# Kernel optimization log

Hardware: AMD Instinct MI355X
Metric: run time of the kernel (lower is better)

## Reference

```python
import jax, jax.numpy as jnp
import numpy as np

B, L, F = 512, 128, 300          # batch, cycles per sample, curve length
D_MODEL = 512
D_LLM = 4096
E = 8                            # num_experts
G = 2                            # num_general_experts
TOP_K = 2
P = TOP_K / E                    # top-p threshold = topK / num_experts
EPS = 1e-9


def setup_inputs() -> dict:
    key = jax.random.key(0)
    ks = jax.random.split(key, 8)
    s_in = 1.0 / np.sqrt(3 * F).astype(np.float32)   # torch Linear init bound
    s_g = 1.0 / np.sqrt(D_LLM).astype(np.float32)
    return {
        "cycle_curve_data": jax.random.normal(ks[0], (B, L, 3, F), jnp.float32),
        "DKP_embeddings": jax.random.normal(ks[1], (B, D_LLM), jnp.float32),
        "W_exp": jax.random.uniform(ks[2], (E, 3 * F, D_MODEL), jnp.float32, -s_in, s_in),
        "b_exp": jax.random.uniform(ks[3], (E, D_MODEL), jnp.float32, -s_in, s_in),
        "W_gen": jax.random.uniform(ks[4], (G, 3 * F, D_MODEL), jnp.float32, -s_in, s_in),
        "b_gen": jax.random.uniform(ks[5], (G, D_MODEL), jnp.float32, -s_in, s_in),
        "W_gate": jax.random.uniform(ks[6], (D_LLM, E), jnp.float32, -s_g, s_g),
        "b_gate": jax.random.uniform(ks[7], (E,), jnp.float32, -s_g, s_g),
    }


def top_p_mask(logits, p):
    # softmax -> sort desc -> cumsum < p (first always kept) -> scatter back
    probs = jax.nn.softmax(logits, axis=-1)
    order = jnp.argsort(-probs, axis=-1)
    cum = jnp.cumsum(jnp.take_along_axis(probs, order, axis=-1), axis=-1)
    m = (cum < p).at[:, 0].set(True)
    rows = jnp.arange(logits.shape[0])[:, None]
    return jnp.zeros(logits.shape, bool).at[rows, order].set(m)


def reference(cycle_curve_data, DKP_embeddings, W_exp, b_exp, W_gen, b_gen, W_gate, b_gate):
    Bsz, Ls = cycle_curve_data.shape[:2]
    x = cycle_curve_data.reshape(Bsz, Ls, -1)            # [B, L, 3F]  (Flatten(start_dim=2))

    # gate (eval path: no noisy gating)
    logits = DKP_embeddings @ W_gate + b_gate            # [B, E]
    mask = top_p_mask(logits, P)
    w = jax.nn.softmax(logits, axis=1) * mask            # masked gate probs
    w = w / (jnp.sum(w, axis=1, keepdims=True) + EPS)    # renormalize (zeros stay zero)

    # dense equivalent of per-expert gather -> Linear -> weighted scatter-combine:
    # tokens with w[b,e]==0 contribute nothing, matching the sparse dispatcher.
    expert_outs = jnp.einsum('blf,efd->ebld', x, W_exp) + b_exp[:, None, None, :]  # [E,B,L,D]
    combined = jnp.einsum('be,ebld->bld', w, expert_outs).astype(jnp.bfloat16)     # [B,L,D] bf16

    # general experts run over the full batch and accumulate (bf16 + f32 -> f32)
    gen = jnp.einsum('blf,gfd->bld', x, W_gen) + jnp.sum(b_gen, axis=0)            # [B,L,D]
    return combined + gen
```

## Files before the change

kernel.cpp:

```cpp
#include <hip/hip_runtime.h>
#include <stdint.h>

#define NB   512
#define NL   128
#define NK   900
#define NKP  928
#define NKT  29
#define ND   512
#define NDLLM 4096
#define NE   8

typedef __bf16 bf16x8 __attribute__((ext_vector_type(8)));
typedef float  f32x4  __attribute__((ext_vector_type(4)));

__device__ __forceinline__ unsigned short f2bf(float f) {
  union { float f; uint32_t u; } v; v.f = f;
  uint32_t u = v.u;
  return (unsigned short)((u + 0x7fffu + ((u >> 16) & 1u)) >> 16);
}

__global__ __launch_bounds__(256) void gate_kernel(
    const float* __restrict__ dkp,
    const float* __restrict__ Wg,
    const float* __restrict__ bg,
    int* __restrict__ eidx)
{
  const int b = blockIdx.x;
  const int t = threadIdx.x;
  float acc[8];
#pragma unroll
  for (int e = 0; e < 8; ++e) acc[e] = 0.f;
  const float* drow = dkp + (size_t)b * NDLLM;
  for (int k = t; k < NDLLM; k += 256) {
    float d = drow[k];
    const float4* w4 = (const float4*)(Wg + (size_t)k * 8);
    float4 w0 = w4[0], w1 = w4[1];
    acc[0] += d * w0.x; acc[1] += d * w0.y; acc[2] += d * w0.z; acc[3] += d * w0.w;
    acc[4] += d * w1.x; acc[5] += d * w1.y; acc[6] += d * w1.z; acc[7] += d * w1.w;
  }
#pragma unroll
  for (int e = 0; e < 8; ++e)
    for (int off = 32; off >= 1; off >>= 1)
      acc[e] += __shfl_down(acc[e], off, 64);

  __shared__ float red[4][8];
  const int wave = t >> 6, lane = t & 63;
  if (lane == 0) {
#pragma unroll
    for (int e = 0; e < 8; ++e) red[wave][e] = acc[e];
  }
  __syncthreads();
  if (t == 0) {
    float best = -1e30f; int bi = 0;
#pragma unroll
    for (int e = 0; e < 8; ++e) {
      float v = red[0][e] + red[1][e] + red[2][e] + red[3][e] + bg[e];
      if (v > best) { best = v; bi = e; }
    }
    eidx[b] = bi;
  }
}

__global__ __launch_bounds__(256) void pack_kernel(
    const float* __restrict__ Wexp,
    const float* __restrict__ Wgen,
    unsigned short* __restrict__ Wt)
{
  const int nt = blockIdx.x;
  const int kt = blockIdx.y;
  const int e  = blockIdx.z;
  const int k0 = kt * 32, n0 = nt * 64;
  __shared__ float tile[32][65];
  const int t = threadIdx.x;
#pragma unroll
  for (int i = 0; i < 8; ++i) {
    int idx = t + i * 256;
    int k = idx >> 6, n = idx & 63;
    int kg = k0 + k;
    float v = 0.f;
    if (kg < NK) {
      size_t off = (size_t)kg * ND + n0 + n;
      v = Wexp[(size_t)e * NK * ND + off] + Wgen[off] + Wgen[(size_t)NK * ND + off];
    }
    tile[k][n] = v;
  }
  __syncthreads();
#pragma unroll
  for (int i = 0; i < 8; ++i) {
    int idx = t + i * 256;
    int n = idx >> 5, k = idx & 31;
    Wt[((size_t)e * ND + n0 + n) * NKP + k0 + k] = f2bf(tile[k][n]);
  }
}

__global__ __launch_bounds__(256) void bias_kernel(
    const float* __restrict__ bexp, const float* __restrict__ bgen,
    float* __restrict__ btot)
{
  int i = blockIdx.x * 256 + threadIdx.x;
  int d = i & (ND - 1);
  btot[i] = bexp[i] + bgen[d] + bgen[ND + d];
}

__global__ __launch_bounds__(256) void gemm_kernel(
    const float* __restrict__ x,
    const unsigned short* __restrict__ Wt,
    const float* __restrict__ btot,
    const int* __restrict__ eidx,
    float* __restrict__ out)
{
  __shared__ unsigned short As[NL * 32];
  __shared__ unsigned short Bs[128 * 32];

  const int b  = blockIdx.y;
  const int nt = blockIdx.x;
  const int t  = threadIdx.x;
  const int lane = t & 63;
  const int w  = t >> 6;
  const int wm = (w >> 1) * 64;
  const int wn = (w & 1) * 64;
  const int ln = lane & 15;
  const int kq = lane >> 4;

  const int e = eidx[b];
  const float* xb = x + (size_t)b * NL * NK;
  const unsigned short* wtb = Wt + ((size_t)e * ND + (size_t)nt * 128) * NKP;

  f32x4 acc[4][4];
  const f32x4 zero = {0.f, 0.f, 0.f, 0.f};
#pragma unroll
  for (int i = 0; i < 4; ++i)
#pragma unroll
    for (int j = 0; j < 4; ++j) acc[i][j] = zero;

  const int al  = t >> 3;
  const int akc = t & 7;

  for (int kt = 0; kt < NKT; ++kt) {
    const int k0 = kt * 32;
    __syncthreads();

#pragma unroll
    for (int p = 0; p < 2; ++p) {
      int c = t + p * 256;
      int n = c >> 2, kc8 = c & 3;
      const unsigned short* src = wtb + (size_t)n * NKP + k0 + kc8 * 8;
      unsigned short* dst = &Bs[c * 8];
      __builtin_amdgcn_global_load_lds(
          (__attribute__((address_space(1))) void*)(void*)src,
          (__attribute__((address_space(3))) void*)dst, 16, 0, 0);
    }

#pragma unroll
    for (int p = 0; p < 4; ++p) {
      int l  = al + p * 32;
      int kg = k0 + akc * 4;
      ushort4 h;
      if (kg < NK) {
        const float4 v = *(const float4*)(xb + (size_t)l * NK + kg);
        h.x = f2bf(v.x); h.y = f2bf(v.y); h.z = f2bf(v.z); h.w = f2bf(v.w);
      } else {
        h.x = 0; h.y = 0; h.z = 0; h.w = 0;
      }
      *(ushort4*)&As[l * 32 + akc * 4] = h;
    }
    __syncthreads();

    bf16x8 af[4], bv[4];
#pragma unroll
    for (int mi = 0; mi < 4; ++mi)
      af[mi] = *(bf16x8*)&As[(wm + mi * 16 + ln) * 32 + kq * 8];
#pragma unroll
    for (int ni = 0; ni < 4; ++ni)
      bv[ni] = *(bf16x8*)&Bs[(wn + ni * 16 + ln) * 32 + kq * 8];
#pragma unroll
    for (int mi = 0; mi < 4; ++mi)
#pragma unroll
      for (int ni = 0; ni < 4; ++ni)
        acc[mi][ni] = __builtin_amdgcn_mfma_f32_16x16x32_bf16(
            af[mi], bv[ni], acc[mi][ni], 0, 0, 0);
  }

  const float* bt = btot + (size_t)e * ND;
  const int nb = nt * 128;
#pragma unroll
  for (int ni = 0; ni < 4; ++ni) {
    int ncol = nb + wn + ni * 16 + ln;
    float bias = bt[ncol];
#pragma unroll
    for (int mi = 0; mi < 4; ++mi) {
      int l0 = wm + mi * 16 + kq * 4;
      float* op = out + ((size_t)b * NL + l0) * ND + ncol;
#pragma unroll
      for (int r = 0; r < 4; ++r)
        op[(size_t)r * ND] = acc[mi][ni][r] + bias;
    }
  }
}

extern "C" void kernel_launch(void* const* d_in, const int* in_sizes, int n_in,
                              void* d_out, int out_size, void* d_ws, size_t ws_size,
                              hipStream_t stream) {
  const float* x     = (const float*)d_in[0];
  const float* dkp   = (const float*)d_in[1];
  const float* Wexp  = (const float*)d_in[2];
  const float* bexp  = (const float*)d_in[3];
  const float* Wgen  = (const float*)d_in[4];
  const float* bgen  = (const float*)d_in[5];
  const float* Wgate = (const float*)d_in[6];
  const float* bgate = (const float*)d_in[7];
  float* out = (float*)d_out;

  int*   eidx = (int*)d_ws;
  float* btot = (float*)((char*)d_ws + 2048);
  unsigned short* Wt = (unsigned short*)((char*)d_ws + 18432);

  gate_kernel<<<NB, 256, 0, stream>>>(dkp, Wgate, bgate, eidx);
  pack_kernel<<<dim3(8, NKT, NE), 256, 0, stream>>>(Wexp, Wgen, Wt);
  bias_kernel<<<16, 256, 0, stream>>>(bexp, bgen, btot);
  gemm_kernel<<<dim3(4, NB), 256, 0, stream>>>(x, Wt, btot, eidx, out);
}
```

Before: 592.2 us.

## Compute full D row per block with double-buffered register-staged LDS pipeline

The GEMM now assigns one block of 512 threads per batch sample, covering all 512 output columns, so each x tile is read and converted to bf16 once instead of four times. Global loads for the next K-step are issued into registers before the MFMA compute on the current LDS buffer, giving software pipelining with two LDS buffers. LDS rows are padded to a stride of 40 to reduce bank conflicts, and outputs use nontemporal stores. The costs are more accumulator registers per thread (128 floats), more LDS per block, a 2-blocks-per-CU launch bound, and a grid of only 512 blocks, which lowers occupancy and parallelism.

```diff
diff --git a/kernel.cpp b/kernel.cpp
--- a/kernel.cpp
+++ b/kernel.cpp
@@ -9,6 +9,7 @@
 #define ND   512
 #define NDLLM 4096
 #define NE   8
+#define ASTR 40
 
 typedef __bf16 bf16x8 __attribute__((ext_vector_type(8)));
 typedef float  f32x4  __attribute__((ext_vector_type(4)));
@@ -102,100 +103,122 @@
   btot[i] = bexp[i] + bgen[d] + bgen[ND + d];
 }
 
-__global__ __launch_bounds__(256) void gemm_kernel(
+__global__ __launch_bounds__(512, 2) void gemm_kernel(
     const float* __restrict__ x,
     const unsigned short* __restrict__ Wt,
     const float* __restrict__ btot,
     const int* __restrict__ eidx,
     float* __restrict__ out)
 {
-  __shared__ unsigned short As[NL * 32];
-  __shared__ unsigned short Bs[128 * 32];
-
-  const int b  = blockIdx.y;
-  const int nt = blockIdx.x;
-  const int t  = threadIdx.x;
+  __shared__ unsigned short As[2][NL * ASTR];
+  __shared__ unsigned short Bs[2][ND * ASTR];
+
+  const int b    = blockIdx.x;
+  const int t    = threadIdx.x;
   const int lane = t & 63;
-  const int w  = t >> 6;
-  const int wm = (w >> 1) * 64;
-  const int wn = (w & 1) * 64;
-  const int ln = lane & 15;
-  const int kq = lane >> 4;
+  const int w    = t >> 6;
+  const int wm   = (w >> 2) * 64;
+  const int wn   = (w & 3) * 128;
+  const int ln   = lane & 15;
+  const int kq   = lane >> 4;
 
   const int e = eidx[b];
   const float* xb = x + (size_t)b * NL * NK;
-  const unsigned short* wtb = Wt + ((size_t)e * ND + (size_t)nt * 128) * NKP;
-
-  f32x4 acc[4][4];
+  const unsigned short* wtb = Wt + (size_t)e * ND * NKP;
+
+  const int arow  = t >> 3;
+  const int acol  = t & 7;
+  const int brow  = t >> 2;
+  const int bslot = t & 3;
+
+  f32x4 acc[4][8];
   const f32x4 zero = {0.f, 0.f, 0.f, 0.f};
 #pragma unroll
-  for (int i = 0; i < 4; ++i)
-#pragma unroll
-    for (int j = 0; j < 4; ++j) acc[i][j] = zero;
-
-  const int al  = t >> 3;
-  const int akc = t & 7;
-
-  for (int kt = 0; kt < NKT; ++kt) {
-    const int k0 = kt * 32;
+  for (int mi = 0; mi < 4; ++mi)
+#pragma unroll
+    for (int ni = 0; ni < 8; ++ni) acc[mi][ni] = zero;
+
+  f32x4 aIn[2];
+  uint4 bIn[4];
+
+#define ISSUE_LOADS(K0)                                                       \
+  {                                                                           \
+    const int kg_ = (K0) + acol * 4;                                          \
+    if (kg_ < NK) {                                                           \
+      aIn[0] = *(const f32x4*)(xb + (size_t)arow * NK + kg_);                 \
+      aIn[1] = *(const f32x4*)(xb + (size_t)(arow + 64) * NK + kg_);          \
+    } else {                                                                  \
+      aIn[0] = zero; aIn[1] = zero;                                           \
+    }                                                                         \
+    const unsigned short* bsrc_ = wtb + (K0) + bslot * 8;                     \
+    _Pragma("unroll")                                                         \
+    for (int p = 0; p < 4; ++p)                                               \
+      bIn[p] = *(const uint4*)(bsrc_ + (size_t)(brow + p * 128) * NKP);       \
+  }
+
+#define WRITE_STAGE(BUF)                                                      \
+  {                                                                           \
+    _Pragma("unroll")                                                         \
+    for (int p = 0; p < 2; ++p) {                                             \
+      ushort4 h_;                                                             \
+      h_.x = f2bf(aIn[p][0]); h_.y = f2bf(aIn[p][1]);                         \
+      h_.z = f2bf(aIn[p][2]); h_.w = f2bf(aIn[p][3]);                         \
+      *(ushort4*)&As[BUF][(arow + p * 64) * ASTR + acol * 4] = h_;            \
+    }                                                                         \
+    _Pragma("unroll")                                                         \
+    for (int p = 0; p < 4; ++p)                                               \
+      *(uint4*)&Bs[BUF][(brow + p * 128) * ASTR + bslot * 8] = bIn[p];        \
+  }
+
+#define COMPUTE(BUF)                                                          \
+  {                                                                           \
+    bf16x8 af_[4];                                                            \
+    _Pragma("unroll")                                                         \
+    for (int mi = 0; mi < 4; ++mi)                                            \
+      af_[mi] = *(bf16x8*)&As[BUF][(wm + mi * 16 + ln) * ASTR + kq * 8];      \
+    _Pragma("unroll")                                                         \
+    for (int ni = 0; ni < 8; ++ni) {                                          \
+      bf16x8 bv_ = *(bf16x8*)&Bs[BUF][(wn + ni * 16 + ln) * ASTR + kq * 8];   \
+      _Pragma("unroll")                                                       \
+      for (int mi = 0; mi < 4; ++mi)                                          \
+        acc[mi][ni] = __builtin_amdgcn_mfma_f32_16x16x32_bf16(                \
+            af_[mi], bv_, acc[mi][ni], 0, 0, 0);                              \
+    }                                                                         \
+  }
+
+  ISSUE_LOADS(0);
+  WRITE_STAGE(0);
+  __syncthreads();
+
+  int cur = 0;
+  for (int kt = 0; kt < NKT - 1; ++kt) {
+    ISSUE_LOADS((kt + 1) * 32);
+    COMPUTE(cur);
     __syncthreads();
-
-#pragma unroll
-    for (int p = 0; p < 2; ++p) {
-      int c = t + p * 256;
-      int n = c >> 2, kc8 = c & 3;
-      const unsigned short* src = wtb + (size_t)n * NKP + k0 + kc8 * 8;
-      unsigned short* dst = &Bs[c * 8];
-      __builtin_amdgcn_global_load_lds(
-          (__attribute__((address_space(1))) void*)(void*)src,
-          (__attribute__((address_space(3))) void*)dst, 16, 0, 0);
+    WRITE_STAGE(cur ^ 1);
+    __syncthreads();
+    cur ^= 1;
+  }
+  COMPUTE(cur);
+
+  const float* bt = btot + (size_t)e * ND;
+#pragma unroll
+  for (int ni = 0; ni < 8; ++ni) {
+    const int ncol = wn + ni * 16 + ln;
+    const float bias = bt[ncol];
+#pragma unroll
+    for (int mi = 0; mi < 4; ++mi) {
+      const int l0 = wm + mi * 16 + kq * 4;
+      float* op = out + ((size_t)b * NL + l0) * ND + ncol;
+#pragma unroll
+      for (int r = 0; r < 4; ++r)
+        __builtin_nontemporal_store(acc[mi][ni][r] + bias, op + (size_t)r * ND);
     }
-
-#pragma unroll
-    for (int p = 0; p < 4; ++p) {
-      int l  = al + p * 32;
-      int kg = k0 + akc * 4;
-      ushort4 h;
-      if (kg < NK) {
-        const float4 v = *(const float4*)(xb + (size_t)l * NK + kg);
-        h.x = f2bf(v.x); h.y = f2bf(v.y); h.z = f2bf(v.z); h.w = f2bf(v.w);
-      } else {
-        h.x = 0; h.y = 0; h.z = 0; h.w = 0;
-      }
-      *(ushort4*)&As[l * 32 + akc * 4] = h;
-    }
-    __syncthreads();
-
-    bf16x8 af[4], bv[4];
-#pragma unroll
-    for (int mi = 0; mi < 4; ++mi)
-      af[mi] = *(bf16x8*)&As[(wm + mi * 16 + ln) * 32 + kq * 8];
-#pragma unroll
-    for (int ni = 0; ni < 4; ++ni)
-      bv[ni] = *(bf16x8*)&Bs[(wn + ni * 16 + ln) * 32 + kq * 8];
-#pragma unroll
-    for (int mi = 0; mi < 4; ++mi)
-#pragma unroll
-      for (int ni = 0; ni < 4; ++ni)
-        acc[mi][ni] = __builtin_amdgcn_mfma_f32_16x16x32_bf16(
-            af[mi], bv[ni], acc[mi][ni], 0, 0, 0);
-  }
-
-  const float* bt = btot + (size_t)e * ND;
-  const int nb = nt * 128;
-#pragma unroll
-  for (int ni = 0; ni < 4; ++ni) {
-    int ncol = nb + wn + ni * 16 + ln;
-    float bias = bt[ncol];
-#pragma unroll
-    for (int mi = 0; mi < 4; ++mi) {
-      int l0 = wm + mi * 16 + kq * 4;
-      float* op = out + ((size_t)b * NL + l0) * ND + ncol;
-#pragma unroll
-      for (int r = 0; r < 4; ++r)
-        op[(size_t)r * ND] = acc[mi][ni][r] + bias;
-    }
-  }
+  }
+
+#undef ISSUE_LOADS
+#undef WRITE_STAGE
+#undef COMPUTE
 }
 
 extern "C" void kernel_launch(void* const* d_in, const int* in_sizes, int n_in,
@@ -218,5 +241,5 @@
   gate_kernel<<<NB, 256, 0, stream>>>(dkp, Wgate, bgate, eidx);
   pack_kernel<<<dim3(8, NKT, NE), 256, 0, stream>>>(Wexp, Wgen, Wt);
   bias_kernel<<<16, 256, 0, stream>>>(bexp, bgen, btot);
-  gemm_kernel<<<dim3(4, NB), 256, 0, stream>>>(x, Wt, btot, eidx, out);
-}
+  gemm_kernel<<<dim3(NB), 512, 0, stream>>>(x, Wt, btot, eidx, out);
+}
```

New measurement: 502.9 us. -15.1%, faster.
